# Performance work log

Hardware: AMD Instinct MI355X
Metric: run time of the kernel (lower is better)

## Reference

```python
import jax, jax.numpy as jnp
import numpy as np

N = 100000; E = 1600000; B = 256; T = 200
EMB = 128; GH = 64; H = 128; DUR = 32; TDIM = 4
IN1 = 2 + EMB + TDIM  # 134


def setup_inputs() -> dict:
    key = jax.random.key(0)
    ks = jax.random.split(key, 20)
    f32 = jnp.float32
    D_IN = EMB + DUR  # 160 lstm input
    return dict(
        x_coords=jax.random.normal(ks[0], (N, 2), f32),
        temporal_features=jax.random.normal(ks[1], (N, TDIM), f32),
        edge_index=jax.random.randint(ks[2], (2, E), 0, N),
        edge_weight=jnp.ones((E,), f32),
        seq=jax.random.randint(ks[3], (B, T), 0, N),
        durations=jax.random.uniform(ks[4], (B, T), f32, 0.0, 30.0),
        lengths=jax.random.randint(ks[5], (B,), 1, T + 1),
        node_emb=jax.random.normal(ks[6], (N, EMB), f32) * 0.02,
        gcn1_W=jax.random.normal(ks[7], (IN1, GH), f32) / np.sqrt(IN1),
        gcn1_b=jnp.zeros((GH,), f32),
        gcn2_W=jax.random.normal(ks[8], (GH, EMB), f32) / np.sqrt(GH),
        gcn2_b=jnp.zeros((EMB,), f32),
        dur_W1=jax.random.normal(ks[9], (1, 16), f32),
        dur_b1=jnp.zeros((16,), f32),
        dur_W2=jax.random.normal(ks[10], (16, DUR), f32) * 0.25,
        dur_b2=jnp.zeros((DUR,), f32),
        lstm_Wih_f=jax.random.normal(ks[11], (4 * H, D_IN), f32) / np.sqrt(D_IN),
        lstm_Whh_f=jax.random.normal(ks[12], (4 * H, H), f32) / np.sqrt(H),
        lstm_b_f=jnp.zeros((4 * H,), f32),
        lstm_Wih_b=jax.random.normal(ks[13], (4 * H, D_IN), f32) / np.sqrt(D_IN),
        lstm_Whh_b=jax.random.normal(ks[14], (4 * H, H), f32) / np.sqrt(H),
        lstm_b_b=jnp.zeros((4 * H,), f32),
        attn_W=jax.random.normal(ks[15], (2 * H, 1), f32) / np.sqrt(2 * H),
        attn_b=jnp.zeros((1,), f32),
        fc_W=jax.random.normal(ks[16], (2 * H, N), f32) / np.sqrt(2 * H),
        fc_b=jnp.zeros((N,), f32),
    )


def gcn_conv(x, W, b, edge_index, edge_weight, n):
    # PyG GCNConv: linear -> symmetric-normalized scatter-add with self-loops -> +bias
    row, col = edge_index[0], edge_index[1]
    loop = jnp.arange(n)
    row = jnp.concatenate([row, loop])
    col = jnp.concatenate([col, loop])
    ew = jnp.concatenate([edge_weight, jnp.ones((n,), x.dtype)])
    deg = jax.ops.segment_sum(ew, col, num_segments=n)
    dis = jnp.where(deg > 0, jax.lax.rsqrt(jnp.maximum(deg, 1e-12)), 0.0)
    norm = dis[row] * ew * dis[col]                 # [E+N]
    xw = x @ W                                      # [N, out]
    out = jax.ops.segment_sum(norm[:, None] * xw[row], col, num_segments=n)
    return out + b


def reverse_padded(x, lengths):
    # reverse each sequence within its valid length (packed-sequence semantics)
    t = jnp.arange(x.shape[1])[None, :]
    idx = jnp.where(t < lengths[:, None], lengths[:, None] - 1 - t, t)
    return jnp.take_along_axis(x, idx[:, :, None], axis=1)


def lstm_dir(x, Wih, Whh, b, mask):
    # x: [B,T,D]; mask: [B,T]; torch gate order i,f,g,o; padded steps freeze state, output 0
    Bz = x.shape[0]
    Hh = Whh.shape[1]
    xg = jnp.einsum('btd,gd->btg', x, Wih) + b      # [B,T,4H]

    def step(carry, inp):
        h, c = carry
        xg_t, m_t = inp
        g = xg_t + h @ Whh.T
        i, f, gg, o = jnp.split(g, 4, axis=-1)
        c_new = jax.nn.sigmoid(f) * c + jax.nn.sigmoid(i) * jnp.tanh(gg)
        h_new = jax.nn.sigmoid(o) * jnp.tanh(c_new)
        m = m_t[:, None]
        return (jnp.where(m, h_new, h), jnp.where(m, c_new, c)), jnp.where(m, h_new, 0.0)

    init = (jnp.zeros((Bz, Hh), x.dtype), jnp.zeros((Bz, Hh), x.dtype))
    _, out = jax.lax.scan(step, init, (xg.swapaxes(0, 1), mask.swapaxes(0, 1)))
    return out.swapaxes(0, 1)                        # [B,T,H]


def reference(x_coords, edge_index, seq, durations, lengths, temporal_features, edge_weight,
              node_emb, gcn1_W, gcn1_b, gcn2_W, gcn2_b,
              dur_W1, dur_b1, dur_W2, dur_b2,
              lstm_Wih_f, lstm_Whh_f, lstm_b_f, lstm_Wih_b, lstm_Whh_b, lstm_b_b,
              attn_W, attn_b, fc_W, fc_b):
    n = x_coords.shape[0]
    feats = jnp.concatenate([x_coords, node_emb, temporal_features], axis=1)  # [N,134]
    z = jax.nn.relu(gcn_conv(feats, gcn1_W, gcn1_b, edge_index, edge_weight, n))
    z = gcn_conv(z, gcn2_W, gcn2_b, edge_index, edge_weight, n)               # [N,EMB]
    seq_emb = z[seq]                                                          # [B,T,EMB]
    dur = jnp.log1p(durations)[..., None]                                     # [B,T,1]
    dur_emb = jax.nn.relu(dur @ dur_W1 + dur_b1) @ dur_W2 + dur_b2            # [B,T,DUR]
    x = jnp.concatenate([seq_emb, dur_emb], axis=-1)                          # [B,T,160]
    mask = jnp.arange(x.shape[1])[None, :] < lengths[:, None]                 # [B,T]
    out_f = lstm_dir(x, lstm_Wih_f, lstm_Whh_f, lstm_b_f, mask)
    out_b = reverse_padded(lstm_dir(reverse_padded(x, lengths), lstm_Wih_b, lstm_Whh_b, lstm_b_b, mask), lengths)
    lstm_out = jnp.concatenate([out_f, out_b], axis=-1)                       # [B,T,2H]
    scores = (lstm_out @ attn_W)[..., 0] + attn_b[0]                          # [B,T]
    scores = jnp.where(mask, scores, -jnp.inf)
    w = jax.nn.softmax(scores, axis=1)[..., None]
    context = jnp.sum(lstm_out * w, axis=1)                                   # [B,2H]
    return context @ fc_W + fc_b                                              # [B,N]
```

## Files before the change

kernel.cpp:

```cpp
#include <hip/hip_runtime.h>
#include <math.h>

#define TSEQ_MAX 256

typedef float v2f __attribute__((ext_vector_type(2)));

__device__ __forceinline__ float sigmf(float x){ return 1.f/(1.f+__expf(-x)); }
__device__ __forceinline__ float tanh_f(float x){ return 1.f - 2.f/(__expf(2.f*x)+1.f); }

__global__ void k_deg_init(float* deg, int N){
    int i = blockIdx.x*256 + threadIdx.x;
    if (i < N) deg[i] = 1.0f;
}
__global__ void k_deg_acc(const int* __restrict__ ei, const float* __restrict__ ew, float* deg, int E){
    int e = blockIdx.x*256 + threadIdx.x;
    if (e < E) atomicAdd(&deg[ei[E + e]], ew[e]);
}
__global__ void k_dis(float* deg, int N){
    int i = blockIdx.x*256 + threadIdx.x;
    if (i < N){ float d = deg[i]; deg[i] = (d > 0.f) ? rsqrtf(fmaxf(d, 1e-12f)) : 0.f; }
}

__global__ void k_count(const int* __restrict__ ei, int* __restrict__ cnt, int E){
    int e = blockIdx.x*256 + threadIdx.x;
    if (e < E) atomicAdd(&cnt[ei[E + e]], 1);
}

__global__ __launch_bounds__(256) void k_scan1(const int* __restrict__ cnt, int* __restrict__ base,
        int* __restrict__ partials, int N){
    __shared__ int sh[256];
    int tid = threadIdx.x;
    int i0 = blockIdx.x*1024 + tid*4;
    int v0=0,v1=0,v2=0,v3=0;
    if (i0+0 < N) v0 = cnt[i0+0];
    if (i0+1 < N) v1 = cnt[i0+1];
    if (i0+2 < N) v2 = cnt[i0+2];
    if (i0+3 < N) v3 = cnt[i0+3];
    int tsum = v0+v1+v2+v3;
    sh[tid] = tsum;
    __syncthreads();
    for (int off = 1; off < 256; off <<= 1){
        int val = (tid >= off) ? sh[tid-off] : 0;
        __syncthreads();
        sh[tid] += val;
        __syncthreads();
    }
    int excl = sh[tid] - tsum;
    if (i0+0 < N) base[i0+0] = excl;
    if (i0+1 < N) base[i0+1] = excl + v0;
    if (i0+2 < N) base[i0+2] = excl + v0 + v1;
    if (i0+3 < N) base[i0+3] = excl + v0 + v1 + v2;
    if (tid == 255) partials[blockIdx.x] = sh[255];
}
__global__ __launch_bounds__(128) void k_scan2(int* partials, int nb){
    __shared__ int sh[128];
    int tid = threadIdx.x;
    int v = (tid < nb) ? partials[tid] : 0;
    sh[tid] = v;
    __syncthreads();
    for (int off = 1; off < 128; off <<= 1){
        int val = (tid >= off) ? sh[tid-off] : 0;
        __syncthreads();
        sh[tid] += val;
        __syncthreads();
    }
    if (tid < nb) partials[tid] = sh[tid] - v;
}
__global__ void k_scan3(int* base, int* cursor, const int* __restrict__ partials, int N, int E){
    int i = blockIdx.x*256 + threadIdx.x;
    if (i < N){
        int v = base[i] + partials[i >> 10];
        base[i] = v; cursor[i] = v;
    }
    if (i == N) base[N] = E;
}
__global__ void k_scatter(const int* __restrict__ ei, const float* __restrict__ ew,
        const float* __restrict__ dis, int* cursor, int2* __restrict__ sorted, int E){
    int e = blockIdx.x*256 + threadIdx.x;
    if (e < E){
        int r = ei[e], c = ei[E + e];
        float nrm = dis[r] * ew[e] * dis[c];
        int pos = atomicAdd(&cursor[c], 1);
        sorted[pos] = make_int2(r, __float_as_int(nrm));
    }
}

__global__ __launch_bounds__(256) void k_xw1(const float* __restrict__ xc, const float* __restrict__ te,
        const float* __restrict__ emb, const float* __restrict__ W1,
        float* __restrict__ xw1, int N){
    __shared__ float Ws[134*64];
    __shared__ float fs[4][136];
    int tid = threadIdx.x;
    for (int i = tid; i < 134*64; i += 256) Ws[i] = W1[i];
    int sub = tid >> 6, lane = tid & 63;
    int node = blockIdx.x*4 + sub;
    if (node < N){
        fs[sub][2+lane]      = emb[node*128 + lane];
        fs[sub][2+64+lane]   = emb[node*128 + 64 + lane];
        if (lane < 2) fs[sub][lane]       = xc[node*2 + lane];
        if (lane < 4) fs[sub][130 + lane] = te[node*4 + lane];
    }
    __syncthreads();
    if (node < N){
        float acc = 0.f;
        #pragma unroll 2
        for (int k = 0; k < 134; k++) acc += fs[sub][k] * Ws[k*64 + lane];
        xw1[node*64 + lane] = acc;
    }
}

template<bool RELU>
__global__ __launch_bounds__(256) void k_gather64(const int2* __restrict__ sorted, const int* __restrict__ base,
        const float* __restrict__ dis, const float* __restrict__ src, const float* __restrict__ b,
        float* __restrict__ outp, int N){
    int node = blockIdx.x*4 + (threadIdx.x >> 6);
    int lane = threadIdx.x & 63;
    if (node >= N) return;
    int s = base[node], e_end = base[node+1];
    float d = dis[node];
    float self = src[(size_t)node*64 + lane];
    if (RELU) self = fmaxf(self, 0.f);
    float acc = d*d*self;
    if (!RELU) acc += b[lane];
    int e = s;
    for (; e + 4 <= e_end; e += 4){
        int2 p0 = sorted[e+0];
        int2 p1 = sorted[e+1];
        int2 p2 = sorted[e+2];
        int2 p3 = sorted[e+3];
        float v0 = src[(size_t)p0.x*64 + lane];
        float v1 = src[(size_t)p1.x*64 + lane];
        float v2 = src[(size_t)p2.x*64 + lane];
        float v3 = src[(size_t)p3.x*64 + lane];
        if (RELU){ v0=fmaxf(v0,0.f); v1=fmaxf(v1,0.f); v2=fmaxf(v2,0.f); v3=fmaxf(v3,0.f); }
        acc += __int_as_float(p0.y)*v0 + __int_as_float(p1.y)*v1
             + __int_as_float(p2.y)*v2 + __int_as_float(p3.y)*v3;
    }
    for (; e < e_end; e++){
        int2 pr = sorted[e];
        float v = src[(size_t)pr.x*64 + lane];
        if (RELU) v = fmaxf(v, 0.f);
        acc += __int_as_float(pr.y)*v;
    }
    outp[(size_t)node*64 + lane] = acc;
}

__global__ __launch_bounds__(256) void k_proj(const float* __restrict__ agg, const float* __restrict__ W2,
        const float* __restrict__ b2, float* __restrict__ z, int N){
    __shared__ float Ws[64*128];
    __shared__ float zs[2][68];
    int tid = threadIdx.x;
    for (int i = tid; i < 64*128; i += 256) Ws[i] = W2[i];
    int sub = tid >> 7, lane = tid & 127;
    float bb = b2[lane];
    #pragma unroll
    for (int p = 0; p < 4; p++){
        int node = blockIdx.x*8 + p*2 + sub;
        __syncthreads();
        if (node < N && lane < 64) zs[sub][lane] = agg[(size_t)node*64 + lane];
        __syncthreads();
        if (node < N){
            float acc = bb;
            #pragma unroll 4
            for (int k = 0; k < 64; k++) acc += zs[sub][k] * Ws[k*128 + lane];
            z[(size_t)node*128 + lane] = acc;
        }
    }
}

__global__ void k_build_x(const float* __restrict__ z, const int* __restrict__ seq,
        const float* __restrict__ dur, const float* __restrict__ dW1, const float* __restrict__ db1,
        const float* __restrict__ dW2, const float* __restrict__ db2, float* __restrict__ x){
    int row = blockIdx.x;
    int tid = threadIdx.x;
    if (tid < 128){
        int node = seq[row];
        x[row*160 + tid] = z[node*128 + tid];
    } else if (tid < 160){
        int jj = tid - 128;
        float ld = log1pf(dur[row]);
        float acc = db2[jj];
        #pragma unroll
        for (int hh = 0; hh < 16; hh++){
            float hv = fmaxf(ld * dW1[hh] + db1[hh], 0.f);
            acc += hv * dW2[hh*32 + jj];
        }
        x[row*160 + tid] = acc;
    }
}

__global__ void k_transpose_wih(const float* __restrict__ Wf, const float* __restrict__ Wb,
        float* __restrict__ Tf, float* __restrict__ Tb){
    int idx = blockIdx.x*256 + threadIdx.x;
    if (idx < 512*160){
        int g = idx / 160, k = idx % 160;
        Tf[k*512 + g] = Wf[idx];
        Tb[k*512 + g] = Wb[idx];
    }
}

#define MT 64
#define NT 128
#define KC 16
__global__ __launch_bounds__(256) void k_gemm(const float* __restrict__ A, const float* __restrict__ B,
        const float* __restrict__ bias, float* __restrict__ C, int M, int Nn, int K){
    __shared__ float As[KC][MT+4];
    __shared__ float Bs[KC][NT+4];
    int tid = threadIdx.x;
    int n0 = blockIdx.x * NT;
    int m0 = blockIdx.y * MT;
    int tn = tid & 31;
    int tm = tid >> 5;
    v2f acc[8][2];
    #pragma unroll
    for (int i = 0; i < 8; i++){ acc[i][0] = (v2f){0.f,0.f}; acc[i][1] = (v2f){0.f,0.f}; }

    for (int kt = 0; kt < K; kt += KC){
        {
            int m = tid >> 2, q = tid & 3;
            float4 a4 = *(const float4*)(A + (size_t)(m0+m)*K + kt + q*4);
            As[q*4+0][m] = a4.x; As[q*4+1][m] = a4.y; As[q*4+2][m] = a4.z; As[q*4+3][m] = a4.w;
        }
        {
            #pragma unroll
            for (int i = 0; i < 2; i++){
                int idx = tid*2 + i;
                int r = idx >> 5, c4 = idx & 31;
                int col = n0 + c4*4;
                float4 bv = make_float4(0.f,0.f,0.f,0.f);
                if (col < Nn) bv = *(const float4*)(B + (size_t)(kt+r)*Nn + col);
                *(float4*)(&Bs[r][c4*4]) = bv;
            }
        }
        __syncthreads();
        #pragma unroll
        for (int k = 0; k < KC; k++){
            float4 b4 = *(const float4*)(&Bs[k][tn*4]);
            v2f b01 = (v2f){b4.x, b4.y};
            v2f b23 = (v2f){b4.z, b4.w};
            float4 a0 = *(const float4*)(&As[k][tm*8]);
            float4 a1 = *(const float4*)(&As[k][tm*8+4]);
            float av[8] = {a0.x,a0.y,a0.z,a0.w,a1.x,a1.y,a1.z,a1.w};
            #pragma unroll
            for (int i = 0; i < 8; i++){
                v2f ai = (v2f){av[i], av[i]};
                acc[i][0] = __builtin_elementwise_fma(ai, b01, acc[i][0]);
                acc[i][1] = __builtin_elementwise_fma(ai, b23, acc[i][1]);
            }
        }
        __syncthreads();
    }
    int col = n0 + tn*4;
    if (col < Nn){
        float4 bb = *(const float4*)(bias + col);
        #pragma unroll
        for (int i = 0; i < 8; i++){
            int row = m0 + tm*8 + i;
            float4 o = make_float4(acc[i][0].x+bb.x, acc[i][0].y+bb.y, acc[i][1].x+bb.z, acc[i][1].y+bb.w);
            *(float4*)(C + (size_t)row*Nn + col) = o;
        }
    }
}

__global__ __launch_bounds__(512) void k_sortjobs(const int* __restrict__ lengths,
        int* __restrict__ jobs, int* __restrict__ counter){
    __shared__ int keys[512];
    __shared__ int vals[512];
    int tid = threadIdx.x;
    keys[tid] = -lengths[tid >> 1];
    vals[tid] = tid;
    __syncthreads();
    for (int k = 2; k <= 512; k <<= 1){
        for (int jj = k >> 1; jj > 0; jj >>= 1){
            int ixj = tid ^ jj;
            if (ixj > tid){
                bool up = ((tid & k) == 0);
                int k0 = keys[tid], k1 = keys[ixj];
                if ((k0 > k1) == up){
                    keys[tid] = k1; keys[ixj] = k0;
                    int v0 = vals[tid]; vals[tid] = vals[ixj]; vals[ixj] = v0;
                }
            }
            __syncthreads();
        }
    }
    jobs[tid] = vals[tid];
    if (tid == 0) *counter = 0;
}

__global__ void __attribute__((amdgpu_flat_work_group_size(1024, 1024), amdgpu_waves_per_eu(4, 4)))
k_lstm(const float* __restrict__ xg_f, const float* __restrict__ xg_b,
        const float* __restrict__ Whh_f, const float* __restrict__ Whh_b,
        const int* __restrict__ lengths, const int* __restrict__ jobs, int* __restrict__ counter,
        float* __restrict__ lstm_out, int T, int NJOBS){
    __shared__ int job_s;
    __shared__ float h_pad[8*24];
    __shared__ float g_lds[512];
    int t = threadIdx.x;
    int Gq = t >> 3;
    int s  = t & 7;
    bool wr = (s < 4);
    int jout = 4*Gq + s;

    for (;;){
        if (t == 0) job_s = atomicAdd(counter, 1);
        __syncthreads();
        int js = job_s;
        if (js >= NJOBS) return;
        int job = jobs[js];
        int b = job >> 1, dir = job & 1;
        const float* xg  = dir ? xg_b  : xg_f;
        const float* Whh = dir ? Whh_b : Whh_f;
        int len = lengths[b];

        v2f w[32];
        const float* wbase = Whh + (size_t)(4*Gq)*128 + 16*s;
        #pragma unroll
        for (int r = 0; r < 4; r++){
            const v2f* wrow = (const v2f*)(wbase + r*128);
            #pragma unroll
            for (int c = 0; c < 8; c++) w[r*8+c] = wrow[c];
        }
        #pragma unroll
        for (int k = 0; k < 32; k++) asm volatile("" : "+v"(w[k]));

        if (t < 128) h_pad[(t>>4)*24 + (t&15)] = 0.f;
        float cst = 0.f;
        const float* xgb = xg + (size_t)b*T*512 + jout;
        float* lob = lstm_out + (size_t)b*T*256 + dir*128 + t;
        float xg_next = 0.f, xg_next2 = 0.f;
        if (wr){
            int t0 = dir ? (len-1) : 0;
            xg_next = xgb[(size_t)t0*512];
            if (len > 1){
                int t1 = dir ? (len-2) : 1;
                xg_next2 = xgb[(size_t)t1*512];
            }
        }
        __syncthreads();

        for (int st = 0; st < len; st++){
            int tt = dir ? (len-1-st) : st;
            float xgv = xg_next;
            xg_next = xg_next2;
            if (wr && st+2 < len){
                int tn = dir ? (len-3-st) : (st+2);
                xg_next2 = xgb[(size_t)tn*512];
            }
            const float4* hp = (const float4*)(h_pad + s*24);
            v2f ac0 = (v2f){0.f,0.f}, ac1 = (v2f){0.f,0.f}, ac2 = (v2f){0.f,0.f}, ac3 = (v2f){0.f,0.f};
            #pragma unroll
            for (int c = 0; c < 4; c++){
                float4 hv = hp[c];
                v2f h01 = (v2f){hv.x, hv.y};
                v2f h23 = (v2f){hv.z, hv.w};
                ac0 = __builtin_elementwise_fma(w[0*8+2*c],   h01, ac0);
                ac0 = __builtin_elementwise_fma(w[0*8+2*c+1], h23, ac0);
                ac1 = __builtin_elementwise_fma(w[1*8+2*c],   h01, ac1);
                ac1 = __builtin_elementwise_fma(w[1*8+2*c+1], h23, ac1);
                ac2 = __builtin_elementwise_fma(w[2*8+2*c],   h01, ac2);
                ac2 = __builtin_elementwise_fma(w[2*8+2*c+1], h23, ac2);
                ac3 = __builtin_elementwise_fma(w[3*8+2*c],   h01, ac3);
                ac3 = __builtin_elementwise_fma(w[3*8+2*c+1], h23, ac3);
            }
            float a0 = ac0.x + ac0.y;
            float a1 = ac1.x + ac1.y;
            float a2 = ac2.x + ac2.y;
            float a3 = ac3.x + ac3.y;
            int s1 = s & 1, s2 = (s >> 1) & 1;
            float b0 = (s1 ? a1 : a0) + __shfl_xor(s1 ? a0 : a1, 1);
            float b1 = (s1 ? a3 : a2) + __shfl_xor(s1 ? a2 : a3, 1);
            float cs = (s2 ? b1 : b0) + __shfl_xor(s2 ? b0 : b1, 2);
            float gsum = cs + __shfl_xor(cs, 4);
            if (wr) g_lds[jout] = gsum + xgv;
            asm volatile("s_waitcnt lgkmcnt(0)" ::: "memory");
            __builtin_amdgcn_s_barrier();
            if (t < 128){
                float gi = g_lds[t], gf = g_lds[128+t], gg = g_lds[256+t], go = g_lds[384+t];
                float cn = sigmf(gf)*cst + sigmf(gi)*tanh_f(gg);
                float hn = sigmf(go)*tanh_f(cn);
                cst = cn;
                h_pad[(t>>4)*24 + (t&15)] = hn;
                lob[(size_t)tt*256] = hn;
            }
            asm volatile("s_waitcnt lgkmcnt(0)" ::: "memory");
            __builtin_amdgcn_s_barrier();
        }
        __syncthreads();
    }
}

__global__ __launch_bounds__(256) void k_attn(const float* __restrict__ lstm_out,
        const float* __restrict__ attn_W, const int* __restrict__ lengths,
        float* __restrict__ context, int T){
    int b = blockIdx.x;
    int tid = threadIdx.x;
    int len = lengths[b];
    __shared__ float sc[TSEQ_MAX];
    __shared__ float red[8];
    int lane = tid & 63, wv = tid >> 6;
    float a0 = attn_W[lane], a1 = attn_W[64+lane], a2 = attn_W[128+lane], a3 = attn_W[192+lane];
    for (int t = wv; t < len; t += 4){
        const float* r = lstm_out + ((size_t)b*T + t)*256;
        float p = r[lane]*a0 + r[64+lane]*a1 + r[128+lane]*a2 + r[192+lane]*a3;
        #pragma unroll
        for (int o = 32; o > 0; o >>= 1) p += __shfl_down(p, o);
        if (lane == 0) sc[t] = p;
    }
    __syncthreads();
    float v = (tid < len) ? sc[tid] : -INFINITY;
    float m = v;
    #pragma unroll
    for (int o = 32; o > 0; o >>= 1) m = fmaxf(m, __shfl_down(m, o));
    if (lane == 0) red[wv] = m;
    __syncthreads();
    float M4 = fmaxf(fmaxf(red[0],red[1]), fmaxf(red[2],red[3]));
    float e = (tid < len) ? __expf(v - M4) : 0.f;
    float ss = e;
    #pragma unroll
    for (int o = 32; o > 0; o >>= 1) ss += __shfl_down(ss, o);
    if (lane == 0) red[4+wv] = ss;
    __syncthreads();
    float S = red[4]+red[5]+red[6]+red[7];
    sc[tid] = e / S;
    __syncthreads();
    float acc = 0.f;
    for (int t = 0; t < len; t++) acc += sc[t] * lstm_out[((size_t)b*T + t)*256 + tid];
    context[b*256 + tid] = acc;
}

extern "C" void kernel_launch(void* const* d_in, const int* in_sizes, int n_in,
                              void* d_out, int out_size, void* d_ws, size_t ws_size,
                              hipStream_t stream) {
    const float* x_coords  = (const float*)d_in[0];
    const float* temporal  = (const float*)d_in[1];
    const int*   edge_idx  = (const int*)  d_in[2];
    const float* edge_w    = (const float*)d_in[3];
    const int*   seq       = (const int*)  d_in[4];
    const float* durations = (const float*)d_in[5];
    const int*   lengths   = (const int*)  d_in[6];
    const float* node_emb  = (const float*)d_in[7];
    const float* gcn1_W    = (const float*)d_in[8];
    const float* gcn1_b    = (const float*)d_in[9];
    const float* gcn2_W    = (const float*)d_in[10];
    const float* gcn2_b    = (const float*)d_in[11];
    const float* dur_W1    = (const float*)d_in[12];
    const float* dur_b1    = (const float*)d_in[13];
    const float* dur_W2    = (const float*)d_in[14];
    const float* dur_b2    = (const float*)d_in[15];
    const float* Wih_f     = (const float*)d_in[16];
    const float* Whh_f     = (const float*)d_in[17];
    const float* b_f       = (const float*)d_in[18];
    const float* Wih_b     = (const float*)d_in[19];
    const float* Whh_b     = (const float*)d_in[20];
    const float* b_b       = (const float*)d_in[21];
    const float* attn_W    = (const float*)d_in[22];
    const float* fc_W      = (const float*)d_in[24];
    const float* fc_b      = (const float*)d_in[25];
    float* out = (float*)d_out;
    float* ws  = (float*)d_ws;

    const int N  = in_sizes[0] / 2;
    const int E  = in_sizes[2] / 2;
    const int B  = in_sizes[6];
    const int T  = in_sizes[4] / B;
    const int BT = B * T;

    float* xg_f     = ws + 0;
    float* xg_b     = ws + 26214400;
    float* xbuf     = ws + 52428800;
    float* lstm_out = ws + 60620800;
    float* context  = ws + 73728000;
    float* WihT_f   = ws + 73793536;
    float* WihT_b   = ws + 73875456;

    int* jobs    = (int*)context;
    int* counter = (int*)context + 512;

    float* dis  = ws + 0;
    float* xw1  = ws + 100352;
    float* out1 = ws + 6500352;
    float* agg  = ws + 12900352;
    float* zbuf = ws + 25700352;
    int2*  sorted   = (int2*)(ws + 38500352);
    int*   cnt      = (int*) (ws + 41700352);
    int*   base     = (int*) (ws + 41800352);
    int*   cursor   = (int*) (ws + 41900356);
    int*   partials = (int*) (ws + 42000356);

    const int SCAN_BLOCKS = (N + 1023) / 1024;

    k_sortjobs<<<dim3(1), dim3(512), 0, stream>>>(lengths, jobs, counter);

    k_deg_init<<<dim3((N+255)/256), dim3(256), 0, stream>>>(dis, N);
    k_deg_acc <<<dim3((E+255)/256), dim3(256), 0, stream>>>(edge_idx, edge_w, dis, E);
    k_dis     <<<dim3((N+255)/256), dim3(256), 0, stream>>>(dis, N);

    hipMemsetAsync(cnt, 0, (size_t)N*sizeof(int), stream);
    k_count  <<<dim3((E+255)/256), dim3(256), 0, stream>>>(edge_idx, cnt, E);
    k_scan1  <<<dim3(SCAN_BLOCKS), dim3(256), 0, stream>>>(cnt, base, partials, N);
    k_scan2  <<<dim3(1), dim3(128), 0, stream>>>(partials, SCAN_BLOCKS);
    k_scan3  <<<dim3((N+256)/256), dim3(256), 0, stream>>>(base, cursor, partials, N, E);
    k_scatter<<<dim3((E+255)/256), dim3(256), 0, stream>>>(edge_idx, edge_w, dis, cursor, sorted, E);

    k_xw1<<<dim3((N+3)/4), dim3(256), 0, stream>>>(x_coords, temporal, node_emb, gcn1_W, xw1, N);
    k_gather64<false><<<dim3((N+3)/4), dim3(256), 0, stream>>>(sorted, base, dis, xw1, gcn1_b, out1, N);

    k_gather64<true><<<dim3((N+3)/4), dim3(256), 0, stream>>>(sorted, base, dis, out1, nullptr, agg, N);
    k_proj<<<dim3((N+7)/8), dim3(256), 0, stream>>>(agg, gcn2_W, gcn2_b, zbuf, N);

    k_build_x<<<dim3(BT), dim3(192), 0, stream>>>(zbuf, seq, durations, dur_W1, dur_b1, dur_W2, dur_b2, xbuf);

    k_transpose_wih<<<dim3(320), dim3(256), 0, stream>>>(Wih_f, Wih_b, WihT_f, WihT_b);
    k_gemm<<<dim3(512/NT, BT/MT), dim3(256), 0, stream>>>(xbuf, WihT_f, b_f, xg_f, BT, 512, 160);
    k_gemm<<<dim3(512/NT, BT/MT), dim3(256), 0, stream>>>(xbuf, WihT_b, b_b, xg_b, BT, 512, 160);

    k_lstm<<<dim3(256), dim3(1024), 0, stream>>>(xg_f, xg_b, Whh_f, Whh_b, lengths, jobs, counter, lstm_out, T, 2*B);

    k_attn<<<dim3(B), dim3(256), 0, stream>>>(lstm_out, attn_W, lengths, context, T);

    k_gemm<<<dim3((N + NT - 1)/NT, B/MT), dim3(256), 0, stream>>>(context, fc_W, fc_b, out, B, N, 256);
}
```

Baseline: 1.499 ms.

## Compute LSTM gates in registers per hidden unit and double-buffer h to drop a barrier

The gate work is remapped so each group of 8 threads owns one hidden unit and its four gate rows. A full xor-shuffle reduction then leaves all four gates in every lane, so the cell update runs in registers without the gate round-trip through LDS. The hidden state is double-buffered in LDS, which cuts the per-timestep barriers from two to one on the serial recurrence. In exchange every thread loads four xg values per step and computes the nonlinearities redundantly, and the shuffle count grows from 4 to 12.

New measurement: 1.631 ms. +8.8%, slower.

```diff
diff --git a/kernel.cpp b/kernel.cpp
--- a/kernel.cpp
+++ b/kernel.cpp
@@ -294,13 +294,11 @@
         const int* __restrict__ lengths, const int* __restrict__ jobs, int* __restrict__ counter,
         float* __restrict__ lstm_out, int T, int NJOBS){
     __shared__ int job_s;
-    __shared__ float h_pad[8*24];
-    __shared__ float g_lds[512];
+    __shared__ float hbuf[2][8*24];
     int t = threadIdx.x;
-    int Gq = t >> 3;
-    int s  = t & 7;
-    bool wr = (s < 4);
-    int jout = 4*Gq + s;
+    int j = t >> 3;
+    int s = t & 7;
+    bool s0 = (s == 0);
 
     for (;;){
         if (t == 0) job_s = atomicAdd(counter, 1);
@@ -313,78 +311,84 @@
         const float* Whh = dir ? Whh_b : Whh_f;
         int len = lengths[b];
 
-        v2f w[32];
-        const float* wbase = Whh + (size_t)(4*Gq)*128 + 16*s;
+        v2f w0[8], w1[8], w2[8], w3[8];
+        {
+            const v2f* r0 = (const v2f*)(Whh + (size_t)(      j)*128 + 16*s);
+            const v2f* r1 = (const v2f*)(Whh + (size_t)(128 + j)*128 + 16*s);
+            const v2f* r2 = (const v2f*)(Whh + (size_t)(256 + j)*128 + 16*s);
+            const v2f* r3 = (const v2f*)(Whh + (size_t)(384 + j)*128 + 16*s);
+            #pragma unroll
+            for (int c = 0; c < 8; c++){ w0[c]=r0[c]; w1[c]=r1[c]; w2[c]=r2[c]; w3[c]=r3[c]; }
+        }
         #pragma unroll
-        for (int r = 0; r < 4; r++){
-            const v2f* wrow = (const v2f*)(wbase + r*128);
-            #pragma unroll
-            for (int c = 0; c < 8; c++) w[r*8+c] = wrow[c];
-        }
-        #pragma unroll
-        for (int k = 0; k < 32; k++) asm volatile("" : "+v"(w[k]));
-
-        if (t < 128) h_pad[(t>>4)*24 + (t&15)] = 0.f;
+        for (int c = 0; c < 8; c++){
+            asm volatile("" : "+v"(w0[c]), "+v"(w1[c]), "+v"(w2[c]), "+v"(w3[c]));
+        }
+
+        if (s0) hbuf[0][(j>>4)*24 + (j&15)] = 0.f;
         float cst = 0.f;
-        const float* xgb = xg + (size_t)b*T*512 + jout;
-        float* lob = lstm_out + (size_t)b*T*256 + dir*128 + t;
-        float xg_next = 0.f, xg_next2 = 0.f;
-        if (wr){
+        const float* xgq = xg + (size_t)b*T*512 + j;
+        float* lob = lstm_out + (size_t)b*T*256 + dir*128 + j;
+        float x0=0,x1=0,x2=0,x3=0, y0=0,y1=0,y2=0,y3=0;
+        {
             int t0 = dir ? (len-1) : 0;
-            xg_next = xgb[(size_t)t0*512];
+            const float* p = xgq + (size_t)t0*512;
+            x0=p[0]; x1=p[128]; x2=p[256]; x3=p[384];
             if (len > 1){
                 int t1 = dir ? (len-2) : 1;
-                xg_next2 = xgb[(size_t)t1*512];
-            }
-        }
-        __syncthreads();
-
+                const float* q = xgq + (size_t)t1*512;
+                y0=q[0]; y1=q[128]; y2=q[256]; y3=q[384];
+            }
+        }
+        __syncthreads();
+
+        int cur = 0;
         for (int st = 0; st < len; st++){
             int tt = dir ? (len-1-st) : st;
-            float xgv = xg_next;
-            xg_next = xg_next2;
-            if (wr && st+2 < len){
+            float xv0=x0, xv1=x1, xv2=x2, xv3=x3;
+            x0=y0; x1=y1; x2=y2; x3=y3;
+            if (st+2 < len){
                 int tn = dir ? (len-3-st) : (st+2);
-                xg_next2 = xgb[(size_t)tn*512];
-            }
-            const float4* hp = (const float4*)(h_pad + s*24);
-            v2f ac0 = (v2f){0.f,0.f}, ac1 = (v2f){0.f,0.f}, ac2 = (v2f){0.f,0.f}, ac3 = (v2f){0.f,0.f};
+                const float* q = xgq + (size_t)tn*512;
+                y0=q[0]; y1=q[128]; y2=q[256]; y3=q[384];
+            }
+            const float4* hp = (const float4*)(&hbuf[cur][s*24]);
+            v2f a0v={0.f,0.f}, a1v={0.f,0.f}, a2v={0.f,0.f}, a3v={0.f,0.f};
             #pragma unroll
             for (int c = 0; c < 4; c++){
                 float4 hv = hp[c];
-                v2f h01 = (v2f){hv.x, hv.y};
-                v2f h23 = (v2f){hv.z, hv.w};
-                ac0 = __builtin_elementwise_fma(w[0*8+2*c],   h01, ac0);
-                ac0 = __builtin_elementwise_fma(w[0*8+2*c+1], h23, ac0);
-                ac1 = __builtin_elementwise_fma(w[1*8+2*c],   h01, ac1);
-                ac1 = __builtin_elementwise_fma(w[1*8+2*c+1], h23, ac1);
-                ac2 = __builtin_elementwise_fma(w[2*8+2*c],   h01, ac2);
-                ac2 = __builtin_elementwise_fma(w[2*8+2*c+1], h23, ac2);
-                ac3 = __builtin_elementwise_fma(w[3*8+2*c],   h01, ac3);
-                ac3 = __builtin_elementwise_fma(w[3*8+2*c+1], h23, ac3);
-            }
-            float a0 = ac0.x + ac0.y;
-            float a1 = ac1.x + ac1.y;
-            float a2 = ac2.x + ac2.y;
-            float a3 = ac3.x + ac3.y;
-            int s1 = s & 1, s2 = (s >> 1) & 1;
-            float b0 = (s1 ? a1 : a0) + __shfl_xor(s1 ? a0 : a1, 1);
-            float b1 = (s1 ? a3 : a2) + __shfl_xor(s1 ? a2 : a3, 1);
-            float cs = (s2 ? b1 : b0) + __shfl_xor(s2 ? b0 : b1, 2);
-            float gsum = cs + __shfl_xor(cs, 4);
-            if (wr) g_lds[jout] = gsum + xgv;
+                v2f hA = (v2f){hv.x, hv.y};
+                v2f hB = (v2f){hv.z, hv.w};
+                a0v = __builtin_elementwise_fma(w0[2*c],   hA, a0v);
+                a0v = __builtin_elementwise_fma(w0[2*c+1], hB, a0v);
+                a1v = __builtin_elementwise_fma(w1[2*c],   hA, a1v);
+                a1v = __builtin_elementwise_fma(w1[2*c+1], hB, a1v);
+                a2v = __builtin_elementwise_fma(w2[2*c],   hA, a2v);
+                a2v = __builtin_elementwise_fma(w2[2*c+1], hB, a2v);
+                a3v = __builtin_elementwise_fma(w3[2*c],   hA, a3v);
+                a3v = __builtin_elementwise_fma(w3[2*c+1], hB, a3v);
+            }
+            float a0 = a0v.x + a0v.y;
+            float a1 = a1v.x + a1v.y;
+            float a2 = a2v.x + a2v.y;
+            float a3 = a3v.x + a3v.y;
+            a0 += __shfl_xor(a0,1); a0 += __shfl_xor(a0,2); a0 += __shfl_xor(a0,4);
+            a1 += __shfl_xor(a1,1); a1 += __shfl_xor(a1,2); a1 += __shfl_xor(a1,4);
+            a2 += __shfl_xor(a2,1); a2 += __shfl_xor(a2,2); a2 += __shfl_xor(a2,4);
+            a3 += __shfl_xor(a3,1); a3 += __shfl_xor(a3,2); a3 += __shfl_xor(a3,4);
+            float gi = a0 + xv0, gf = a1 + xv1, gg = a2 + xv2, go = a3 + xv3;
+            float cn = sigmf(gf)*cst + sigmf(gi)*tanh_f(gg);
+            float hn = sigmf(go)*tanh_f(cn);
+            cst = cn;
+            int nxt = cur ^ 1;
+            if (s0){
+                hbuf[nxt][(j>>4)*24 + (j&15)] = hn;
+                lob[(size_t)tt*256] = hn;
+            }
             asm volatile("s_waitcnt lgkmcnt(0)" ::: "memory");
             __builtin_amdgcn_s_barrier();
-            if (t < 128){
-                float gi = g_lds[t], gf = g_lds[128+t], gg = g_lds[256+t], go = g_lds[384+t];
-                float cn = sigmf(gf)*cst + sigmf(gi)*tanh_f(gg);
-                float hn = sigmf(go)*tanh_f(cn);
-                cst = cn;
-                h_pad[(t>>4)*24 + (t&15)] = hn;
-                lob[(size_t)tt*256] = hn;
-            }
-            asm volatile("s_waitcnt lgkmcnt(0)" ::: "memory");
-            __builtin_amdgcn_s_barrier();
+            asm volatile("" ::: "memory");
+            cur = nxt;
         }
         __syncthreads();
     }
```
